# Kernel optimization log

Measured on AMD Instinct MI355X. Metric: run time of the kernel, lower is better.

## Reference

```python
import jax, jax.numpy as jnp
import numpy as np

B, N, D = 8, 4096, 512


def setup_inputs() -> dict:
    key = jax.random.key(0)
    k1, k2 = jax.random.split(key)
    tgt = jax.random.normal(k1, (B, N, D), dtype=jnp.float32)
    query_pos = jax.random.normal(k2, (B, N, D), dtype=jnp.float32)
    objects_num = N  # scalar int, unused by the math (as in the torch module)
    return {"tgt": tgt, "query_pos": query_pos, "objects_num": objects_num}


def reference(tgt, query_pos, objects_num):
    # L2-normalize along feature dim (torch .norm default: 2-norm, no eps)
    tgt_norm = tgt / jnp.linalg.norm(tgt, axis=-1, keepdims=True)
    # cosine similarity matrix [B, N, N]
    sim = jnp.einsum("bnd,bmd->bnm", tgt_norm, tgt_norm)
    # elementwise tanh, then re-aggregate original (un-normalized) tgt
    out = jnp.einsum("bnm,bmd->bnd", jnp.tanh(sim), tgt)
    return out
```

## Files before the change

### kernel.cpp

```cpp
#include <hip/hip_runtime.h>
#include <hip/hip_bf16.h>

#define B_ 8
#define N_ 4096
#define D_ 512
#define BM 64
#define BK 64
#define NTH 512
#define NT (N_ / BK)

typedef __attribute__((ext_vector_type(8))) short bf16x8;
typedef __attribute__((ext_vector_type(4))) float f32x4;
typedef __attribute__((ext_vector_type(16))) float f32x16;

__device__ __forceinline__ short f2bs(float x) {
  union { __hip_bfloat16 h; short s; } u;
  u.h = __float2bfloat16(x);
  return u.s;
}

__device__ __forceinline__ void gld16(const void* g, void* l) {
  __builtin_amdgcn_global_load_lds((const __attribute__((address_space(1))) void*)g,
                                   (__attribute__((address_space(3))) void*)l, 16, 0, 0);
}

__global__ void __launch_bounds__(256) rnorm_kernel(const float* __restrict__ tgt,
                                                    float* __restrict__ rn) {
  int row  = blockIdx.x * 4 + (threadIdx.x >> 6);
  int lane = threadIdx.x & 63;
  const float* p = tgt + (size_t)row * D_ + lane * 8;
  float4 a = *(const float4*)p;
  float4 b = *(const float4*)(p + 4);
  float s = a.x*a.x + a.y*a.y + a.z*a.z + a.w*a.w
          + b.x*b.x + b.y*b.y + b.z*b.z + b.w*b.w;
  #pragma unroll
  for (int m = 32; m >= 1; m >>= 1) s += __shfl_xor(s, m, 64);
  if (lane == 0) rn[row] = rsqrtf(s);
}

__global__ void __launch_bounds__(256) prep_kernel(const float* __restrict__ tgt,
                                                   const float* __restrict__ rn,
                                                   ushort* __restrict__ Tbf2,
                                                   ushort* __restrict__ Vt2) {
  __shared__ ushort L[64][72];
  const int id = blockIdx.x;
  const int b = id >> 9, nt = (id >> 3) & 63, dt = id & 7;
  const int n0 = nt * 64, d0 = dt * 64;
  const int t = threadIdx.x;
  const float* Tg  = tgt + ((size_t)b * N_ + n0) * D_ + d0;
  const float* rnb = rn + b * N_ + n0;
  ushort* T2 = Tbf2 + (size_t)b * N_ * D_;
  ushort* V2 = Vt2  + (size_t)b * N_ * D_;

  const int r = t >> 3, g = t & 7;
  #pragma unroll
  for (int p = 0; p < 2; ++p) {
    int row = p * 32 + r;
    const float* src = Tg + (size_t)row * D_ + g * 8;
    float4 f0 = *(const float4*)src;
    float4 f1 = *(const float4*)(src + 4);
    float sc = rnb[row];
    bf16x8 nv;
    nv[0]=f2bs(f0.x*sc); nv[1]=f2bs(f0.y*sc); nv[2]=f2bs(f0.z*sc); nv[3]=f2bs(f0.w*sc);
    nv[4]=f2bs(f1.x*sc); nv[5]=f2bs(f1.y*sc); nv[6]=f2bs(f1.z*sc); nv[7]=f2bs(f1.w*sc);
    *(bf16x8*)(T2 + ((size_t)(d0/8 + g) * N_ + n0 + row) * 8) = nv;
    bf16x8 rv;
    rv[0]=f2bs(f0.x); rv[1]=f2bs(f0.y); rv[2]=f2bs(f0.z); rv[3]=f2bs(f0.w);
    rv[4]=f2bs(f1.x); rv[5]=f2bs(f1.y); rv[6]=f2bs(f1.z); rv[7]=f2bs(f1.w);
    #pragma unroll
    for (int e = 0; e < 8; ++e) L[row][g*8 + e] = (ushort)rv[e];
  }
  __syncthreads();
  #pragma unroll
  for (int p = 0; p < 2; ++p) {
    int task = p * 256 + t;
    int ng = task >> 6, dd = task & 63;
    bf16x8 v;
    #pragma unroll
    for (int j = 0; j < 8; ++j) v[j] = (short)L[ng*8 + j][dd];
    *(bf16x8*)(V2 + ((size_t)(n0/8 + ng) * D_ + d0 + dd) * 8) = v;
  }
}

__global__ void __launch_bounds__(NTH, 2) fused_kernel(const ushort* __restrict__ Tbf2,
                                                       const ushort* __restrict__ Vt2,
                                                       float* __restrict__ out) {
  __shared__ __align__(16) ushort KV[BK * D_];
  __shared__ __align__(16) ushort VT[BK * D_];
  __shared__ __align__(16) ushort Pl[BM * BK];

  const int id = blockIdx.x;
  const int b  = id & 7;
  const int q0 = (id >> 3) * BM;

  const int lane = threadIdx.x & 63;
  const int w    = threadIdx.x >> 6;

  const ushort* Tb2 = Tbf2 + (size_t)b * N_ * D_;
  const ushort* Vb2 = Vt2  + (size_t)b * N_ * D_;

  const int qG = w >> 1;
  const int mG = w & 1;

  bf16x8 qf[16];
  {
    const int row = q0 + qG * 16 + (lane & 15);
    #pragma unroll
    for (int kk = 0; kk < 16; ++kk) {
      int g = kk * 4 + (lane >> 4);
      qf[kk] = *(const bf16x8*)(Tb2 + ((size_t)g * N_ + row) * 8);
    }
  }

  f32x16 acc[2][2] = {};

  const ushort* kvrd = &KV[(lane >> 4) * 512 + (mG * 32 + (lane & 15)) * 8];
  const ushort* pard = &Pl[(lane >> 5) * 512 + (lane & 31) * 8];
  const ushort* vbrd = &VT[(lane >> 5) * 4096 + (w * 64 + (lane & 31)) * 8];
  ushort*       plwr = &Pl[((mG * 32 + (lane & 15)) >> 3) * 512
                           + (qG * 16 + (lane >> 4) * 4) * 8
                           + ((lane & 15) & 7)];

  const ushort* kvsrc = Tb2 + (size_t)(w * 8) * N_ * 8 + (size_t)BK * 8 + lane * 8;
  const ushort* vtsrc = Vb2 + (size_t)(8 + w) * D_ * 8 + lane * 8;

  #pragma unroll
  for (int i = 0; i < 8; ++i)
    gld16(Tb2 + ((size_t)(w * 8 + i) * N_) * 8 + lane * 8, &KV[(w * 8 + i) * 512]);
  #pragma unroll
  for (int i = 0; i < 8; ++i)
    gld16(Vb2 + (size_t)w * D_ * 8 + i * 512 + lane * 8, &VT[w * 4096 + i * 512]);
  __syncthreads();

  for (int t = 0; t < NT; ++t) {
    f32x4 sacc[2] = {};
    __builtin_amdgcn_s_setprio(1);
    #pragma unroll
    for (int kk = 0; kk < 16; ++kk) {
      bf16x8 b0 = *(const bf16x8*)(kvrd + kk * 2048);
      bf16x8 b1 = *(const bf16x8*)(kvrd + kk * 2048 + 128);
      sacc[0] = __builtin_amdgcn_mfma_f32_16x16x32_bf16(qf[kk], b0, sacc[0], 0, 0, 0);
      sacc[1] = __builtin_amdgcn_mfma_f32_16x16x32_bf16(qf[kk], b1, sacc[1], 0, 0, 0);
    }
    __builtin_amdgcn_s_setprio(0);

    #pragma unroll
    for (int f = 0; f < 2; ++f)
      #pragma unroll
      for (int j = 0; j < 4; ++j) {
        float e = __builtin_amdgcn_exp2f(sacc[f][j] * 2.885390082f);
        float tn = 1.0f - 2.0f * __builtin_amdgcn_rcpf(e + 1.0f);
        plwr[f * 1024 + j * 8] = (ushort)f2bs(tn);
      }
    __syncthreads();

    if (t < NT - 1) {
      #pragma unroll
      for (int i = 0; i < 8; ++i)
        gld16(kvsrc + (size_t)i * N_ * 8, &KV[(w * 8 + i) * 512]);
      kvsrc += BK * 8;
    }

    __builtin_amdgcn_s_setprio(1);
    #pragma unroll
    for (int ks = 0; ks < 4; ++ks) {
      bf16x8 pa0 = *(const bf16x8*)(pard + ks * 1024);
      bf16x8 pa1 = *(const bf16x8*)(pard + ks * 1024 + 256);
      bf16x8 vb0 = *(const bf16x8*)(vbrd + ks * 8192);
      bf16x8 vb1 = *(const bf16x8*)(vbrd + ks * 8192 + 256);
      acc[0][0] = __builtin_amdgcn_mfma_f32_32x32x16_bf16(pa0, vb0, acc[0][0], 0, 0, 0);
      acc[0][1] = __builtin_amdgcn_mfma_f32_32x32x16_bf16(pa0, vb1, acc[0][1], 0, 0, 0);
      acc[1][0] = __builtin_amdgcn_mfma_f32_32x32x16_bf16(pa1, vb0, acc[1][0], 0, 0, 0);
      acc[1][1] = __builtin_amdgcn_mfma_f32_32x32x16_bf16(pa1, vb1, acc[1][1], 0, 0, 0);
    }
    __builtin_amdgcn_s_setprio(0);
    __syncthreads();

    if (t < NT - 1) {
      #pragma unroll
      for (int i = 0; i < 8; ++i)
        gld16(vtsrc + i * 512, &VT[w * 4096 + i * 512]);
      vtsrc += 8 * D_ * 8;
    }
  }

  {
    float* op = out + (size_t)b * N_ * D_ + (size_t)q0 * D_;
    #pragma unroll
    for (int qs = 0; qs < 2; ++qs)
      #pragma unroll
      for (int ds = 0; ds < 2; ++ds) {
        int d = w * 64 + ds * 32 + (lane & 31);
        #pragma unroll
        for (int reg = 0; reg < 16; ++reg) {
          int row = qs * 32 + (reg & 3) + 8 * (reg >> 2) + 4 * (lane >> 5);
          op[(size_t)row * D_ + d] = acc[qs][ds][reg];
        }
      }
  }
}

extern "C" void kernel_launch(void* const* d_in, const int* in_sizes, int n_in,
                              void* d_out, int out_size, void* d_ws, size_t ws_size,
                              hipStream_t stream) {
  const float* tgt = (const float*)d_in[0];
  float* outp = (float*)d_out;

  float*  rn   = (float*)d_ws;
  ushort* Tbf2 = (ushort*)((char*)d_ws + (1 << 17));
  ushort* Vt2  = Tbf2 + (size_t)B_ * N_ * D_;

  rnorm_kernel<<<dim3((B_ * N_) / 4), dim3(256), 0, stream>>>(tgt, rn);
  prep_kernel<<<dim3(B_ * 64 * 8), dim3(256), 0, stream>>>(tgt, rn, Tbf2, Vt2);
  fused_kernel<<<dim3(B_ * (N_ / BM)), dim3(NTH), 0, stream>>>(Tbf2, Vt2, outp);
}
```

Before: 348.6 us.

## Double-buffer K tiles in LDS and load V fragments directly into registers

```diff
diff --git a/kernel.cpp b/kernel.cpp
--- a/kernel.cpp
+++ b/kernel.cpp
@@ -85,8 +85,7 @@
 __global__ void __launch_bounds__(NTH, 2) fused_kernel(const ushort* __restrict__ Tbf2,
                                                        const ushort* __restrict__ Vt2,
                                                        float* __restrict__ out) {
-  __shared__ __align__(16) ushort KV[BK * D_];
-  __shared__ __align__(16) ushort VT[BK * D_];
+  __shared__ __align__(16) ushort KV[2][BK * D_];
   __shared__ __align__(16) ushort Pl[BM * BK];
 
   const int id = blockIdx.x;
@@ -114,25 +113,38 @@
 
   f32x16 acc[2][2] = {};
 
-  const ushort* kvrd = &KV[(lane >> 4) * 512 + (mG * 32 + (lane & 15)) * 8];
-  const ushort* pard = &Pl[(lane >> 5) * 512 + (lane & 31) * 8];
-  const ushort* vbrd = &VT[(lane >> 5) * 4096 + (w * 64 + (lane & 31)) * 8];
-  ushort*       plwr = &Pl[((mG * 32 + (lane & 15)) >> 3) * 512
-                           + (qG * 16 + (lane >> 4) * 4) * 8
-                           + ((lane & 15) & 7)];
-
-  const ushort* kvsrc = Tb2 + (size_t)(w * 8) * N_ * 8 + (size_t)BK * 8 + lane * 8;
-  const ushort* vtsrc = Vb2 + (size_t)(8 + w) * D_ * 8 + lane * 8;
+  const ushort* kvrdA = &KV[0][(lane >> 4) * 512 + (mG * 32 + (lane & 15)) * 8];
+  const ushort* kvrdB = &KV[1][(lane >> 4) * 512 + (mG * 32 + (lane & 15)) * 8];
+  const ushort* pard  = &Pl[(lane >> 5) * 512 + (lane & 31) * 8];
+  ushort*       plwr  = &Pl[((mG * 32 + (lane & 15)) >> 3) * 512
+                            + (qG * 16 + (lane >> 4) * 4) * 8 + (lane & 7)];
+
+  const ushort* kvnext = Tb2 + ((size_t)(w * 8) * N_ + BK) * 8 + lane * 8;
+  const ushort* vbase  = Vb2 + ((size_t)(lane >> 5) * D_ + w * 64 + (lane & 31)) * 8;
 
   #pragma unroll
   for (int i = 0; i < 8; ++i)
-    gld16(Tb2 + ((size_t)(w * 8 + i) * N_) * 8 + lane * 8, &KV[(w * 8 + i) * 512]);
-  #pragma unroll
-  for (int i = 0; i < 8; ++i)
-    gld16(Vb2 + (size_t)w * D_ * 8 + i * 512 + lane * 8, &VT[w * 4096 + i * 512]);
+    gld16(Tb2 + ((size_t)(w * 8 + i) * N_) * 8 + lane * 8, &KV[0][(w * 8 + i) * 512]);
   __syncthreads();
 
   for (int t = 0; t < NT; ++t) {
+    bf16x8 vr[4][2];
+    #pragma unroll
+    for (int ks = 0; ks < 4; ++ks) {
+      vr[ks][0] = *(const bf16x8*)(vbase + (size_t)ks * 2 * D_ * 8);
+      vr[ks][1] = *(const bf16x8*)(vbase + (size_t)ks * 2 * D_ * 8 + 32 * 8);
+    }
+    vbase += (size_t)8 * D_ * 8;
+
+    if (t < NT - 1) {
+      ushort* dst = &KV[(t + 1) & 1][w * 8 * 512];
+      #pragma unroll
+      for (int i = 0; i < 8; ++i)
+        gld16(kvnext + (size_t)i * N_ * 8, dst + i * 512);
+      kvnext += BK * 8;
+    }
+
+    const ushort* kvrd = (t & 1) ? kvrdB : kvrdA;
     f32x4 sacc[2] = {};
     __builtin_amdgcn_s_setprio(1);
     #pragma unroll
@@ -154,34 +166,18 @@
       }
     __syncthreads();
 
-    if (t < NT - 1) {
-      #pragma unroll
-      for (int i = 0; i < 8; ++i)
-        gld16(kvsrc + (size_t)i * N_ * 8, &KV[(w * 8 + i) * 512]);
-      kvsrc += BK * 8;
-    }
-
     __builtin_amdgcn_s_setprio(1);
     #pragma unroll
     for (int ks = 0; ks < 4; ++ks) {
       bf16x8 pa0 = *(const bf16x8*)(pard + ks * 1024);
       bf16x8 pa1 = *(const bf16x8*)(pard + ks * 1024 + 256);
-      bf16x8 vb0 = *(const bf16x8*)(vbrd + ks * 8192);
-      bf16x8 vb1 = *(const bf16x8*)(vbrd + ks * 8192 + 256);
-      acc[0][0] = __builtin_amdgcn_mfma_f32_32x32x16_bf16(pa0, vb0, acc[0][0], 0, 0, 0);
-      acc[0][1] = __builtin_amdgcn_mfma_f32_32x32x16_bf16(pa0, vb1, acc[0][1], 0, 0, 0);
-      acc[1][0] = __builtin_amdgcn_mfma_f32_32x32x16_bf16(pa1, vb0, acc[1][0], 0, 0, 0);
-      acc[1][1] = __builtin_amdgcn_mfma_f32_32x32x16_bf16(pa1, vb1, acc[1][1], 0, 0, 0);
+      acc[0][0] = __builtin_amdgcn_mfma_f32_32x32x16_bf16(pa0, vr[ks][0], acc[0][0], 0, 0, 0);
+      acc[0][1] = __builtin_amdgcn_mfma_f32_32x32x16_bf16(pa0, vr[ks][1], acc[0][1], 0, 0, 0);
+      acc[1][0] = __builtin_amdgcn_mfma_f32_32x32x16_bf16(pa1, vr[ks][0], acc[1][0], 0, 0, 0);
+      acc[1][1] = __builtin_amdgcn_mfma_f32_32x32x16_bf16(pa1, vr[ks][1], acc[1][1], 0, 0, 0);
     }
     __builtin_amdgcn_s_setprio(0);
     __syncthreads();
-
-    if (t < NT - 1) {
-      #pragma unroll
-      for (int i = 0; i < 8; ++i)
-        gld16(vtsrc + i * 512, &VT[w * 4096 + i * 512]);
-      vtsrc += 8 * D_ * 8;
-    }
   }
 
   {
```

Result: slower. 413.9 us (+18.7%).
